# Kernel optimization log

Hardware: AMD Instinct MI355X
Metric: run time of the kernel (lower is better)

## Reference

```python
import jax, jax.numpy as jnp
import numpy as np

B, L, H, O = 2048, 256, 512, 1  # batch, input_len, hidden_size, output_size
EPS = 1e-5

def setup_inputs() -> dict:
    key = jax.random.key(0)
    ks = jax.random.split(key, 16)
    s = 0.05
    return {
        "x": jax.random.normal(ks[0], (B, 1, O), jnp.float32),
        "hidden": jax.random.normal(ks[1], (1, B, H), jnp.float32),
        "encoder_outputs": jax.random.normal(ks[2], (B, L, H), jnp.float32),
        # weights stored [in, out] (transposed torch Linear convention)
        "emb_W": jax.random.normal(ks[3], (O, H), jnp.float32) * s,
        "emb_b": jax.random.normal(ks[4], (H,), jnp.float32) * s,
        "attn_W": jax.random.normal(ks[5], (2 * H, L), jnp.float32) * s,
        "attn_b": jax.random.normal(ks[6], (L,), jnp.float32) * s,
        "comb_W": jax.random.normal(ks[7], (2 * H, H), jnp.float32) * s,
        "comb_b": jax.random.normal(ks[8], (H,), jnp.float32) * s,
        "gru_Wih": jax.random.normal(ks[9], (H, 3 * H), jnp.float32) * s,
        "gru_Whh": jax.random.normal(ks[10], (H, 3 * H), jnp.float32) * s,
        "gru_bih": jax.random.normal(ks[11], (3 * H,), jnp.float32) * s,
        "gru_bhh": jax.random.normal(ks[12], (3 * H,), jnp.float32) * s,
        "out_W": jax.random.normal(ks[13], (H, O), jnp.float32) * s,
        "out_b": jax.random.normal(ks[14], (O,), jnp.float32) * s,
    }

def reference(x, hidden, encoder_outputs, emb_W, emb_b, attn_W, attn_b,
              comb_W, comb_b, gru_Wih, gru_Whh, gru_bih, gru_bhh, out_W, out_b):
    # embedding + InstanceNorm1d over hidden dim (C=1 channel, length=H), no affine
    embedded = x @ emb_W + emb_b                      # [B,1,H]
    mu = jnp.mean(embedded, axis=-1, keepdims=True)
    var = jnp.var(embedded, axis=-1, keepdims=True)   # biased var, matches torch
    embedded = (embedded - mu) * jax.lax.rsqrt(var + EPS)
    # dropout = identity (inference)
    h_b = jnp.transpose(hidden, (1, 0, 2))            # [B,1,H]
    attn_logits = jnp.concatenate([embedded, h_b], axis=2) @ attn_W + attn_b  # [B,1,L]
    attn_weights = jax.nn.softmax(attn_logits, axis=2)
    attn_applied = jnp.einsum('bql,bld->bqd', attn_weights, encoder_outputs)  # [B,1,H]
    out = jnp.concatenate([embedded, attn_applied], axis=2) @ comb_W + comb_b
    out = jax.nn.relu(out)                            # [B,1,H]
    # single GRU step (num_layers=1, seq_len=1)
    xt = out[:, 0, :]                                 # [B,H]
    h0 = hidden[0]                                    # [B,H]
    gi = xt @ gru_Wih + gru_bih                       # [B,3H]
    gh = h0 @ gru_Whh + gru_bhh
    i_r, i_z, i_n = jnp.split(gi, 3, axis=-1)
    h_r, h_z, h_n = jnp.split(gh, 3, axis=-1)
    r = jax.nn.sigmoid(i_r + h_r)
    z = jax.nn.sigmoid(i_z + h_z)
    n = jnp.tanh(i_n + r * h_n)
    h_new = (1.0 - z) * n + z * h0                    # [B,H]
    output = h_new[:, None, :] @ out_W + out_b        # [B,1,O]
    return output, h_new[None, :, :], attn_weights
```

## Files before the change

### kernel.cpp

```cpp
#include <hip/hip_runtime.h>
#include <math.h>

#define NB 2048
#define NL 256
#define NH 512

typedef unsigned short ushort_t;
typedef short s16x8 __attribute__((ext_vector_type(8)));
typedef short s16x4 __attribute__((ext_vector_type(4)));
typedef float f32x4 __attribute__((ext_vector_type(4)));

__device__ __forceinline__ float wsum(float v){
  #pragma unroll
  for (int o = 32; o; o >>= 1) v += __shfl_xor(v, o);
  return v;
}
__device__ __forceinline__ float wmax(float v){
  #pragma unroll
  for (int o = 32; o; o >>= 1) v = fmaxf(v, __shfl_xor(v, o));
  return v;
}
__device__ __forceinline__ ushort_t f2bf(float f){
  union { float f; unsigned u; } v; v.f = f;
  unsigned r = v.u + 0x7fffu + ((v.u >> 16) & 1u);
  return (ushort_t)(r >> 16);
}
__device__ __forceinline__ float bf2f(short s){
  union { unsigned u; float f; } v; v.u = ((unsigned)(unsigned short)s) << 16;
  return v.f;
}

__global__ __launch_bounds__(256)
void kPrep(const float* __restrict__ eW, const float* __restrict__ eb,
           const float* __restrict__ attn_W, const float* __restrict__ comb_W,
           float* __restrict__ stats,
           float* __restrict__ p, float* __restrict__ q,
           float* __restrict__ p2, float* __restrict__ q2)
{
  __shared__ float rw[4], rb[4];
  __shared__ float pa[4][64], pb[4][64];
  const int tid = threadIdx.x, lane = tid & 63, wv = tid >> 6;
  const int bid = blockIdx.x;
  float swv = eW[tid] + eW[tid + 256];
  float sbv = eb[tid] + eb[tid + 256];
  swv = wsum(swv); sbv = wsum(sbv);
  if (lane == 0) { rw[wv] = swv; rb[wv] = sbv; }
  __syncthreads();
  const float mW = (rw[0]+rw[1]+rw[2]+rw[3]) * (1.f/NH);
  const float mb = (rb[0]+rb[1]+rb[2]+rb[3]) * (1.f/NH);

  if (bid == 12) {
    float u0 = eW[tid]-mW, u1 = eW[tid+256]-mW;
    float v0 = eb[tid]-mb, v1 = eb[tid+256]-mb;
    float s2 = u0*u0 + u1*u1, s3 = u0*v0 + u1*v1, s4 = v0*v0 + v1*v1;
    s2 = wsum(s2); s3 = wsum(s3); s4 = wsum(s4);
    if (lane == 0) { pa[0][wv] = s2; pa[1][wv] = s3; pa[2][wv] = s4; }
    __syncthreads();
    if (tid == 0) {
      stats[0] = mW; stats[1] = mb;
      stats[2] = pa[0][0]+pa[0][1]+pa[0][2]+pa[0][3];
      stats[3] = pa[1][0]+pa[1][1]+pa[1][2]+pa[1][3];
      stats[4] = pa[2][0]+pa[2][1]+pa[2][2]+pa[2][3];
    }
    return;
  }
  const float* Wsrc; int ldw, c0; float *op, *oq;
  if (bid < 4) { Wsrc = attn_W; ldw = NL; c0 = bid*64;     op = p  + c0; oq = q  + c0; }
  else         { Wsrc = comb_W; ldw = NH; c0 = (bid-4)*64; op = p2 + c0; oq = q2 + c0; }
  const int c = c0 + lane;
  const int hc = tid >> 6;
  float ap = 0.f, aq = 0.f;
  for (int h = hc*128; h < hc*128 + 128; ++h) {
    float w = Wsrc[(size_t)h*ldw + c];
    ap = fmaf(eW[h]-mW, w, ap);
    aq = fmaf(eb[h]-mb, w, aq);
  }
  pa[hc][lane] = ap; pb[hc][lane] = aq;
  __syncthreads();
  if (hc == 0) {
    op[lane] = pa[0][lane]+pa[1][lane]+pa[2][lane]+pa[3][lane];
    oq[lane] = pb[0][lane]+pb[1][lane]+pb[2][lane]+pb[3][lane];
  }
}

__global__ __launch_bounds__(256)
void kPrepB(const float* __restrict__ hidden,
            const float* __restrict__ attn_W, const float* __restrict__ comb_W,
            const float* __restrict__ Wih, const float* __restrict__ Whh,
            ushort_t* __restrict__ A2, ushort_t* __restrict__ WTA,
            ushort_t* __restrict__ WTC, ushort_t* __restrict__ WTG)
{
  const int bid = blockIdx.x, tid = threadIdx.x;
  if (bid < 512) {
    const int idx = (bid*256 + tid) * 8;
    const int b = idx >> 9, h = idx & 511;
    float4 v0 = *(const float4*)(hidden + idx);
    float4 v1 = *(const float4*)(hidden + idx + 4);
    s16x8 o;
    o[0]=f2bf(v0.x); o[1]=f2bf(v0.y); o[2]=f2bf(v0.z); o[3]=f2bf(v0.w);
    o[4]=f2bf(v1.x); o[5]=f2bf(v1.y); o[6]=f2bf(v1.z); o[7]=f2bf(v1.w);
    *(s16x8*)&A2[(size_t)b*1024 + 512 + h] = o;
    return;
  }
  if (bid < 544) {
    const int b2 = bid - 512, bx = b2 & 3, by = b2 >> 2;
    const int c = bx*64 + (tid & 63);
    const int ksub = by*64 + (tid >> 6)*16;
    ushort_t vals[16];
    #pragma unroll
    for (int kk = 0; kk < 16; ++kk)
      vals[kk] = f2bf(attn_W[(size_t)(512 + ksub + kk)*NL + c]);
    *(s16x8*)&WTA[(size_t)c*512 + ksub]     = *(s16x8*)&vals[0];
    *(s16x8*)&WTA[(size_t)c*512 + ksub + 8] = *(s16x8*)&vals[8];
    return;
  }
  if (bid < 608) {
    const int b2 = bid - 544, bx = b2 & 7, by = b2 >> 3;
    const int c = bx*64 + (tid & 63);
    const int ksub = by*64 + (tid >> 6)*16;
    ushort_t vals[16];
    #pragma unroll
    for (int kk = 0; kk < 16; ++kk)
      vals[kk] = f2bf(comb_W[(size_t)(512 + ksub + kk)*NH + c]);
    *(s16x8*)&WTC[(size_t)c*512 + ksub]     = *(s16x8*)&vals[0];
    *(s16x8*)&WTC[(size_t)c*512 + ksub + 8] = *(s16x8*)&vals[8];
    return;
  }
  {
    const int b2 = bid - 608, bx = b2 & 31, by = b2 >> 5;
    const int n = bx*64 + (tid & 63);
    const int ksub = by*64 + (tid >> 6)*16;
    const int g = n >> 6, t = (n >> 4) & 3, c = (g << 4) | (n & 15);
    const int sc = (t == 0) ? c : (t == 1) ? (512 + c) : (1024 + c);
    ushort_t vals[16];
    #pragma unroll
    for (int kk = 0; kk < 16; ++kk) {
      int k = ksub + kk;
      float v;
      if (k < 512) v = (t == 3) ? 0.f : Wih[(size_t)k*1536 + sc];
      else         v = (t == 2) ? 0.f : Whh[(size_t)(k-512)*1536 + sc];
      vals[kk] = f2bf(v);
    }
    *(s16x8*)&WTG[(size_t)n*1024 + ksub]     = *(s16x8*)&vals[0];
    *(s16x8*)&WTG[(size_t)n*1024 + ksub + 8] = *(s16x8*)&vals[8];
  }
}

__global__ __launch_bounds__(128)
void k2fused(const float* __restrict__ x, const float* __restrict__ hidden,
             const float* __restrict__ enc, const ushort_t* __restrict__ WTA,
             const float* __restrict__ attn_b,
             const float* __restrict__ p, const float* __restrict__ q,
             const float* __restrict__ stats,
             float* __restrict__ attn_out, ushort_t* __restrict__ abf)
{
  __shared__ __align__(16) float h0s[NH];
  __shared__ float wl[NL];
  __shared__ float sred[2];
  const int tid = threadIdx.x, lane = tid & 63, wv = tid >> 6;
  const int b = blockIdx.x;

  ((float4*)h0s)[tid] = ((const float4*)(hidden + (size_t)b*NH))[tid];
  __syncthreads();

  const float xv = x[b];
  const float rs = rsqrtf((xv*xv*stats[2] + 2.f*xv*stats[3] + stats[4])*(1.0f/NH) + 1e-5f);
  float lg[2];
  #pragma unroll
  for (int cc = 0; cc < 2; ++cc) {
    const int c = tid + cc*128;
    const ushort_t* wrow = WTA + (size_t)c*512;
    float acc = 0.f;
    #pragma unroll 4
    for (int k = 0; k < NH; k += 8) {
      s16x8 w = *(const s16x8*)&wrow[k];
      #pragma unroll
      for (int jj = 0; jj < 8; ++jj)
        acc = fmaf(bf2f(w[jj]), h0s[k+jj], acc);
    }
    lg[cc] = acc + attn_b[c] + xv*rs*p[c] + rs*q[c];
  }
  float m = wmax(fmaxf(lg[0], lg[1]));
  if (lane == 0) sred[wv] = m;
  __syncthreads();
  m = fmaxf(sred[0], sred[1]);
  __syncthreads();
  float e0 = expf(lg[0]-m), e1 = expf(lg[1]-m);
  float s = wsum(e0 + e1);
  if (lane == 0) sred[wv] = s;
  __syncthreads();
  const float inv = 1.f / (sred[0] + sred[1]);
  e0 *= inv; e1 *= inv;
  wl[tid] = e0; wl[tid+128] = e1;
  attn_out[(size_t)b*NL + tid]       = e0;
  attn_out[(size_t)b*NL + tid + 128] = e1;
  __syncthreads();

  const float4* ep = (const float4*)(enc + (size_t)b*NL*NH);
  float4 acc = {0.f,0.f,0.f,0.f};
  #pragma unroll 4
  for (int l = 0; l < NL; ++l) {
    float wv2 = wl[l];
    float4 e = ep[l*(NH/4) + tid];
    acc.x = fmaf(wv2,e.x,acc.x); acc.y = fmaf(wv2,e.y,acc.y);
    acc.z = fmaf(wv2,e.z,acc.z); acc.w = fmaf(wv2,e.w,acc.w);
  }
  s16x4 o; o[0]=f2bf(acc.x); o[1]=f2bf(acc.y); o[2]=f2bf(acc.z); o[3]=f2bf(acc.w);
  *(s16x4*)&abf[(size_t)b*NH + tid*4] = o;
}

template<int EPI>
__global__ __launch_bounds__(256)
void gemm_bf16(const ushort_t* __restrict__ A, int lda,
               const ushort_t* __restrict__ Bt, int K,
               const float* __restrict__ xin, const float* __restrict__ stats,
               const float* __restrict__ pvec, const float* __restrict__ qvec,
               const float* __restrict__ bias,
               ushort_t* __restrict__ out_bf,
               const float* __restrict__ bih, const float* __restrict__ bhh,
               const float* __restrict__ hidden, float* __restrict__ h_out)
{
  __shared__ ushort_t As[128][72];
  __shared__ ushort_t Bs[64][72];
  const int tid = threadIdx.x, lane = tid & 63, wr = tid >> 6;
  const int m0 = blockIdx.x * 128, n0 = blockIdx.y * 64;

  f32x4 acc[2][4];
  #pragma unroll
  for (int i = 0; i < 2; ++i)
    #pragma unroll
    for (int j = 0; j < 4; ++j)
      acc[i][j] = (f32x4){0.f,0.f,0.f,0.f};

  const int srow = tid >> 3, scol = (tid & 7) * 8;
  for (int kt = 0; kt < K; kt += 64) {
    __syncthreads();
    #pragma unroll
    for (int it = 0; it < 4; ++it) {
      const int r = srow + it*32;
      *(s16x8*)&As[r][scol] = *(const s16x8*)&A[(size_t)(m0+r)*lda + kt + scol];
    }
    #pragma unroll
    for (int it = 0; it < 2; ++it) {
      const int r = srow + it*32;
      *(s16x8*)&Bs[r][scol] = *(const s16x8*)&Bt[(size_t)(n0+r)*K + kt + scol];
    }
    __syncthreads();
    #pragma unroll
    for (int ks = 0; ks < 2; ++ks) {
      const int ko = ks*32 + (lane >> 4)*8;
      s16x8 af[2], bfr[4];
      #pragma unroll
      for (int i = 0; i < 2; ++i) af[i]  = *(const s16x8*)&As[wr*32 + i*16 + (lane & 15)][ko];
      #pragma unroll
      for (int j = 0; j < 4; ++j) bfr[j] = *(const s16x8*)&Bs[j*16 + (lane & 15)][ko];
      #pragma unroll
      for (int i = 0; i < 2; ++i)
        #pragma unroll
        for (int j = 0; j < 4; ++j)
          acc[i][j] = __builtin_amdgcn_mfma_f32_16x16x32_bf16(af[i], bfr[j], acc[i][j], 0, 0, 0);
    }
  }

  if constexpr (EPI == 2) {
    const float S2 = stats[2], S3 = stats[3], S4 = stats[4];
    #pragma unroll
    for (int i = 0; i < 2; ++i) {
      #pragma unroll
      for (int reg = 0; reg < 4; ++reg) {
        const int row = m0 + wr*32 + i*16 + ((lane >> 4) << 2) + reg;
        const float xv = xin[row];
        const float rs = rsqrtf((xv*xv*S2 + 2.f*xv*S3 + S4)*(1.0f/NH) + 1e-5f);
        const float al = xv*rs, be = rs;
        #pragma unroll
        for (int j = 0; j < 4; ++j) {
          const int col = n0 + j*16 + (lane & 15);
          float v = acc[i][j][reg] + bias[col] + al*pvec[col] + be*qvec[col];
          out_bf[(size_t)row*1024 + col] = f2bf(fmaxf(v, 0.f));
        }
      }
    }
  } else {
    const int g = n0 >> 6;
    const int hcol = (g << 4) | (lane & 15);
    const float b_r = bih[hcol]        + bhh[hcol];
    const float b_z = bih[512 + hcol]  + bhh[512 + hcol];
    const float b_i = bih[1024 + hcol];
    const float b_h = bhh[1024 + hcol];
    #pragma unroll
    for (int i = 0; i < 2; ++i) {
      #pragma unroll
      for (int reg = 0; reg < 4; ++reg) {
        const int row = m0 + wr*32 + i*16 + ((lane >> 4) << 2) + reg;
        float rv = 1.f / (1.f + expf(-(acc[i][0][reg] + b_r)));
        float zv = 1.f / (1.f + expf(-(acc[i][1][reg] + b_z)));
        float nv = tanhf(acc[i][2][reg] + b_i + rv * (acc[i][3][reg] + b_h));
        float h0v = hidden[(size_t)row*NH + hcol];
        h_out[(size_t)row*NH + hcol] = nv + zv * (h0v - nv);
      }
    }
  }
}

__global__ __launch_bounds__(256)
void kOut(const float* __restrict__ h, const float* __restrict__ out_W,
          const float* __restrict__ out_b, float* __restrict__ out0)
{
  const int row = blockIdx.x * 4 + (threadIdx.x >> 6);
  const int lane = threadIdx.x & 63;
  const float4* hp = (const float4*)(h + (size_t)row*NH);
  const float4* wp = (const float4*)out_W;
  float4 h1 = hp[lane*2], h2 = hp[lane*2+1];
  float4 w1 = wp[lane*2], w2 = wp[lane*2+1];
  float d = h1.x*w1.x + h1.y*w1.y + h1.z*w1.z + h1.w*w1.w
          + h2.x*w2.x + h2.y*w2.y + h2.z*w2.z + h2.w*w2.w;
  d = wsum(d);
  if (lane == 0) out0[row] = d + out_b[0];
}

extern "C" void kernel_launch(void* const* d_in, const int* in_sizes, int n_in,
                              void* d_out, int out_size, void* d_ws, size_t ws_size,
                              hipStream_t stream)
{
  const float* x      = (const float*)d_in[0];
  const float* hidden = (const float*)d_in[1];
  const float* enc    = (const float*)d_in[2];
  const float* emb_W  = (const float*)d_in[3];
  const float* emb_b  = (const float*)d_in[4];
  const float* attn_W = (const float*)d_in[5];
  const float* attn_b = (const float*)d_in[6];
  const float* comb_W = (const float*)d_in[7];
  const float* comb_b = (const float*)d_in[8];
  const float* Wih    = (const float*)d_in[9];
  const float* Whh    = (const float*)d_in[10];
  const float* bih    = (const float*)d_in[11];
  const float* bhh    = (const float*)d_in[12];
  const float* out_W  = (const float*)d_in[13];
  const float* out_b  = (const float*)d_in[14];

  float* out      = (float*)d_out;
  float* out0     = out;
  float* out_h    = out + NB;
  float* out_attn = out + NB + (size_t)NB*NH;

  float* wsf   = (float*)d_ws;
  float* stats = wsf;
  float* p     = wsf + 16;
  float* q     = wsf + 272;
  float* p2    = wsf + 528;
  float* q2    = wsf + 1040;
  ushort_t* usb = (ushort_t*)(wsf + 1600);
  ushort_t* A2  = usb;
  ushort_t* ABF = usb + 2097152;
  ushort_t* WTA = usb + 3145728;
  ushort_t* WTC = usb + 3276800;
  ushort_t* WTG = usb + 3538944;

  kPrep<<<13, 256, 0, stream>>>(emb_W, emb_b, attn_W, comb_W, stats, p, q, p2, q2);
  kPrepB<<<1120, 256, 0, stream>>>(hidden, attn_W, comb_W, Wih, Whh, A2, WTA, WTC, WTG);
  k2fused<<<NB, 128, 0, stream>>>(x, hidden, enc, WTA, attn_b, p, q, stats,
                                  out_attn, ABF);
  gemm_bf16<2><<<dim3(16, 8), 256, 0, stream>>>(ABF, 512, WTC, 512,
      x, stats, p2, q2, comb_b, A2, nullptr, nullptr, nullptr, nullptr);
  gemm_bf16<3><<<dim3(16, 32), 256, 0, stream>>>(A2, 1024, WTG, 1024,
      nullptr, nullptr, nullptr, nullptr, nullptr, nullptr, bih, bhh, hidden, out_h);
  kOut<<<512, 256, 0, stream>>>(out_h, out_W, out_b, out0);
}
```

Before: 299.0 us.

## Fuse combine matmul into attention kernel and merge prep kernels

Merges the two prep kernels into one launch. The combine-layer matmul moves into the per-batch attention kernel as an fp32 matrix-vector product over shared-memory attention output, removing the separate bf16 GEMM launch and its intermediate buffer. The attention and combine weights are now kept in fp32 instead of bf16. This cuts launches and intermediate traffic but does 512x512 FMA per row on scalar ALUs, and every block re-reads 1 MB of fp32 combine weights (served from cache), in place of an MFMA GEMM.

Result: slower. 534.5 us (+78.8%).

```diff
diff --git a/kernel.cpp b/kernel.cpp
--- a/kernel.cpp
+++ b/kernel.cpp
@@ -25,70 +25,17 @@
   unsigned r = v.u + 0x7fffu + ((v.u >> 16) & 1u);
   return (ushort_t)(r >> 16);
 }
-__device__ __forceinline__ float bf2f(short s){
-  union { unsigned u; float f; } v; v.u = ((unsigned)(unsigned short)s) << 16;
-  return v.f;
-}
 
 __global__ __launch_bounds__(256)
-void kPrep(const float* __restrict__ eW, const float* __restrict__ eb,
-           const float* __restrict__ attn_W, const float* __restrict__ comb_W,
-           float* __restrict__ stats,
-           float* __restrict__ p, float* __restrict__ q,
-           float* __restrict__ p2, float* __restrict__ q2)
-{
-  __shared__ float rw[4], rb[4];
-  __shared__ float pa[4][64], pb[4][64];
-  const int tid = threadIdx.x, lane = tid & 63, wv = tid >> 6;
-  const int bid = blockIdx.x;
-  float swv = eW[tid] + eW[tid + 256];
-  float sbv = eb[tid] + eb[tid + 256];
-  swv = wsum(swv); sbv = wsum(sbv);
-  if (lane == 0) { rw[wv] = swv; rb[wv] = sbv; }
-  __syncthreads();
-  const float mW = (rw[0]+rw[1]+rw[2]+rw[3]) * (1.f/NH);
-  const float mb = (rb[0]+rb[1]+rb[2]+rb[3]) * (1.f/NH);
-
-  if (bid == 12) {
-    float u0 = eW[tid]-mW, u1 = eW[tid+256]-mW;
-    float v0 = eb[tid]-mb, v1 = eb[tid+256]-mb;
-    float s2 = u0*u0 + u1*u1, s3 = u0*v0 + u1*v1, s4 = v0*v0 + v1*v1;
-    s2 = wsum(s2); s3 = wsum(s3); s4 = wsum(s4);
-    if (lane == 0) { pa[0][wv] = s2; pa[1][wv] = s3; pa[2][wv] = s4; }
-    __syncthreads();
-    if (tid == 0) {
-      stats[0] = mW; stats[1] = mb;
-      stats[2] = pa[0][0]+pa[0][1]+pa[0][2]+pa[0][3];
-      stats[3] = pa[1][0]+pa[1][1]+pa[1][2]+pa[1][3];
-      stats[4] = pa[2][0]+pa[2][1]+pa[2][2]+pa[2][3];
-    }
-    return;
-  }
-  const float* Wsrc; int ldw, c0; float *op, *oq;
-  if (bid < 4) { Wsrc = attn_W; ldw = NL; c0 = bid*64;     op = p  + c0; oq = q  + c0; }
-  else         { Wsrc = comb_W; ldw = NH; c0 = (bid-4)*64; op = p2 + c0; oq = q2 + c0; }
-  const int c = c0 + lane;
-  const int hc = tid >> 6;
-  float ap = 0.f, aq = 0.f;
-  for (int h = hc*128; h < hc*128 + 128; ++h) {
-    float w = Wsrc[(size_t)h*ldw + c];
-    ap = fmaf(eW[h]-mW, w, ap);
-    aq = fmaf(eb[h]-mb, w, aq);
-  }
-  pa[hc][lane] = ap; pb[hc][lane] = aq;
-  __syncthreads();
-  if (hc == 0) {
-    op[lane] = pa[0][lane]+pa[1][lane]+pa[2][lane]+pa[3][lane];
-    oq[lane] = pb[0][lane]+pb[1][lane]+pb[2][lane]+pb[3][lane];
-  }
-}
-
-__global__ __launch_bounds__(256)
-void kPrepB(const float* __restrict__ hidden,
-            const float* __restrict__ attn_W, const float* __restrict__ comb_W,
-            const float* __restrict__ Wih, const float* __restrict__ Whh,
-            ushort_t* __restrict__ A2, ushort_t* __restrict__ WTA,
-            ushort_t* __restrict__ WTC, ushort_t* __restrict__ WTG)
+void kPrepAll(const float* __restrict__ hidden,
+              const float* __restrict__ eW, const float* __restrict__ eb,
+              const float* __restrict__ attn_W, const float* __restrict__ comb_W,
+              const float* __restrict__ Wih, const float* __restrict__ Whh,
+              ushort_t* __restrict__ A2, float* __restrict__ WTA,
+              float* __restrict__ WTC, ushort_t* __restrict__ WTG,
+              float* __restrict__ stats,
+              float* __restrict__ p, float* __restrict__ q,
+              float* __restrict__ p2, float* __restrict__ q2)
 {
   const int bid = blockIdx.x, tid = threadIdx.x;
   if (bid < 512) {
@@ -106,27 +53,29 @@
     const int b2 = bid - 512, bx = b2 & 3, by = b2 >> 2;
     const int c = bx*64 + (tid & 63);
     const int ksub = by*64 + (tid >> 6)*16;
-    ushort_t vals[16];
+    float vals[16];
     #pragma unroll
     for (int kk = 0; kk < 16; ++kk)
-      vals[kk] = f2bf(attn_W[(size_t)(512 + ksub + kk)*NL + c]);
-    *(s16x8*)&WTA[(size_t)c*512 + ksub]     = *(s16x8*)&vals[0];
-    *(s16x8*)&WTA[(size_t)c*512 + ksub + 8] = *(s16x8*)&vals[8];
+      vals[kk] = attn_W[(size_t)(512 + ksub + kk)*NL + c];
+    #pragma unroll
+    for (int kk = 0; kk < 4; ++kk)
+      *(float4*)&WTA[(size_t)c*512 + ksub + kk*4] = *(float4*)&vals[kk*4];
     return;
   }
   if (bid < 608) {
     const int b2 = bid - 544, bx = b2 & 7, by = b2 >> 3;
     const int c = bx*64 + (tid & 63);
     const int ksub = by*64 + (tid >> 6)*16;
-    ushort_t vals[16];
+    float vals[16];
     #pragma unroll
     for (int kk = 0; kk < 16; ++kk)
-      vals[kk] = f2bf(comb_W[(size_t)(512 + ksub + kk)*NH + c]);
-    *(s16x8*)&WTC[(size_t)c*512 + ksub]     = *(s16x8*)&vals[0];
-    *(s16x8*)&WTC[(size_t)c*512 + ksub + 8] = *(s16x8*)&vals[8];
+      vals[kk] = comb_W[(size_t)(512 + ksub + kk)*NH + c];
+    #pragma unroll
+    for (int kk = 0; kk < 4; ++kk)
+      *(float4*)&WTC[(size_t)c*512 + ksub + kk*4] = *(float4*)&vals[kk*4];
     return;
   }
-  {
+  if (bid < 1120) {
     const int b2 = bid - 608, bx = b2 & 31, by = b2 >> 5;
     const int n = bx*64 + (tid & 63);
     const int ksub = by*64 + (tid >> 6)*16;
@@ -143,20 +92,72 @@
     }
     *(s16x8*)&WTG[(size_t)n*1024 + ksub]     = *(s16x8*)&vals[0];
     *(s16x8*)&WTG[(size_t)n*1024 + ksub + 8] = *(s16x8*)&vals[8];
+    return;
+  }
+  {
+    __shared__ float rw[4], rb[4];
+    __shared__ float pa[4][64], pb[4][64];
+    const int lane = tid & 63, wv = tid >> 6;
+    float swv = eW[tid] + eW[tid + 256];
+    float sbv = eb[tid] + eb[tid + 256];
+    swv = wsum(swv); sbv = wsum(sbv);
+    if (lane == 0) { rw[wv] = swv; rb[wv] = sbv; }
+    __syncthreads();
+    const float mW = (rw[0]+rw[1]+rw[2]+rw[3]) * (1.f/NH);
+    const float mb = (rb[0]+rb[1]+rb[2]+rb[3]) * (1.f/NH);
+
+    if (bid == 1132) {
+      float u0 = eW[tid]-mW, u1 = eW[tid+256]-mW;
+      float v0 = eb[tid]-mb, v1 = eb[tid+256]-mb;
+      float s2 = u0*u0 + u1*u1, s3 = u0*v0 + u1*v1, s4 = v0*v0 + v1*v1;
+      s2 = wsum(s2); s3 = wsum(s3); s4 = wsum(s4);
+      if (lane == 0) { pa[0][wv] = s2; pa[1][wv] = s3; pa[2][wv] = s4; }
+      __syncthreads();
+      if (tid == 0) {
+        stats[0] = mW; stats[1] = mb;
+        stats[2] = pa[0][0]+pa[0][1]+pa[0][2]+pa[0][3];
+        stats[3] = pa[1][0]+pa[1][1]+pa[1][2]+pa[1][3];
+        stats[4] = pa[2][0]+pa[2][1]+pa[2][2]+pa[2][3];
+      }
+      return;
+    }
+    const int bid2 = bid - 1120;
+    const float* Wsrc; int ldw, c0; float *op, *oq;
+    if (bid2 < 4) { Wsrc = attn_W; ldw = NL; c0 = bid2*64;     op = p  + c0; oq = q  + c0; }
+    else          { Wsrc = comb_W; ldw = NH; c0 = (bid2-4)*64; op = p2 + c0; oq = q2 + c0; }
+    const int c = c0 + lane;
+    const int hc = tid >> 6;
+    float ap = 0.f, aq = 0.f;
+    #pragma unroll 4
+    for (int h = hc*128; h < hc*128 + 128; ++h) {
+      float w = Wsrc[(size_t)h*ldw + c];
+      ap = fmaf(eW[h]-mW, w, ap);
+      aq = fmaf(eb[h]-mb, w, aq);
+    }
+    pa[hc][lane] = ap; pb[hc][lane] = aq;
+    __syncthreads();
+    if (hc == 0) {
+      op[lane] = pa[0][lane]+pa[1][lane]+pa[2][lane]+pa[3][lane];
+      oq[lane] = pb[0][lane]+pb[1][lane]+pb[2][lane]+pb[3][lane];
+    }
   }
 }
 
 __global__ __launch_bounds__(128)
 void k2fused(const float* __restrict__ x, const float* __restrict__ hidden,
-             const float* __restrict__ enc, const ushort_t* __restrict__ WTA,
-             const float* __restrict__ attn_b,
+             const float* __restrict__ enc,
+             const float* __restrict__ WTA, const float* __restrict__ attn_b,
              const float* __restrict__ p, const float* __restrict__ q,
+             const float* __restrict__ WTC, const float* __restrict__ comb_b,
+             const float* __restrict__ p2, const float* __restrict__ q2,
              const float* __restrict__ stats,
-             float* __restrict__ attn_out, ushort_t* __restrict__ abf)
+             float* __restrict__ attn_out, ushort_t* __restrict__ A2)
 {
   __shared__ __align__(16) float h0s[NH];
+  __shared__ __align__(16) float a_s[NH];
   __shared__ float wl[NL];
   __shared__ float sred[2];
+  __shared__ __align__(16) ushort_t xt_s[NH];
   const int tid = threadIdx.x, lane = tid & 63, wv = tid >> 6;
   const int b = blockIdx.x;
 
@@ -165,20 +166,21 @@
 
   const float xv = x[b];
   const float rs = rsqrtf((xv*xv*stats[2] + 2.f*xv*stats[3] + stats[4])*(1.0f/NH) + 1e-5f);
+  const float al = xv*rs, be = rs;
+
   float lg[2];
   #pragma unroll
   for (int cc = 0; cc < 2; ++cc) {
     const int c = tid + cc*128;
-    const ushort_t* wrow = WTA + (size_t)c*512;
+    const float4* wrow = (const float4*)(WTA + (size_t)c*512);
     float acc = 0.f;
-    #pragma unroll 4
-    for (int k = 0; k < NH; k += 8) {
-      s16x8 w = *(const s16x8*)&wrow[k];
-      #pragma unroll
-      for (int jj = 0; jj < 8; ++jj)
-        acc = fmaf(bf2f(w[jj]), h0s[k+jj], acc);
-    }
-    lg[cc] = acc + attn_b[c] + xv*rs*p[c] + rs*q[c];
+    #pragma unroll 8
+    for (int kq = 0; kq < 128; ++kq) {
+      float4 w = wrow[kq];
+      const float* h4 = &h0s[kq*4];
+      acc = fmaf(w.x,h4[0],fmaf(w.y,h4[1],fmaf(w.z,h4[2],fmaf(w.w,h4[3],acc))));
+    }
+    lg[cc] = acc + attn_b[c] + al*p[c] + be*q[c];
   }
   float m = wmax(fmaxf(lg[0], lg[1]));
   if (lane == 0) sred[wv] = m;
@@ -205,25 +207,37 @@
     acc.x = fmaf(wv2,e.x,acc.x); acc.y = fmaf(wv2,e.y,acc.y);
     acc.z = fmaf(wv2,e.z,acc.z); acc.w = fmaf(wv2,e.w,acc.w);
   }
-  s16x4 o; o[0]=f2bf(acc.x); o[1]=f2bf(acc.y); o[2]=f2bf(acc.z); o[3]=f2bf(acc.w);
-  *(s16x4*)&abf[(size_t)b*NH + tid*4] = o;
-}
-
-template<int EPI>
+  ((float4*)a_s)[tid] = acc;
+  __syncthreads();
+
+  #pragma unroll
+  for (int cc = 0; cc < 4; ++cc) {
+    const int c = tid + cc*128;
+    const float4* wrow = (const float4*)(WTC + (size_t)c*512);
+    const float4* a4 = (const float4*)a_s;
+    float acc2 = comb_b[c] + al*p2[c] + be*q2[c];
+    #pragma unroll 8
+    for (int kq = 0; kq < 128; ++kq) {
+      float4 w = wrow[kq];
+      float4 av = a4[kq];
+      acc2 = fmaf(w.x,av.x,fmaf(w.y,av.y,fmaf(w.z,av.z,fmaf(w.w,av.w,acc2))));
+    }
+    xt_s[c] = f2bf(fmaxf(acc2, 0.f));
+  }
+  __syncthreads();
+  *(s16x4*)&A2[(size_t)b*1024 + tid*4] = *(s16x4*)&xt_s[tid*4];
+}
+
 __global__ __launch_bounds__(256)
-void gemm_bf16(const ushort_t* __restrict__ A, int lda,
-               const ushort_t* __restrict__ Bt, int K,
-               const float* __restrict__ xin, const float* __restrict__ stats,
-               const float* __restrict__ pvec, const float* __restrict__ qvec,
-               const float* __restrict__ bias,
-               ushort_t* __restrict__ out_bf,
-               const float* __restrict__ bih, const float* __restrict__ bhh,
-               const float* __restrict__ hidden, float* __restrict__ h_out)
+void gemmGRU(const ushort_t* __restrict__ A, const ushort_t* __restrict__ Bt,
+             const float* __restrict__ bih, const float* __restrict__ bhh,
+             const float* __restrict__ hidden, float* __restrict__ h_out)
 {
   __shared__ ushort_t As[128][72];
   __shared__ ushort_t Bs[64][72];
   const int tid = threadIdx.x, lane = tid & 63, wr = tid >> 6;
   const int m0 = blockIdx.x * 128, n0 = blockIdx.y * 64;
+  const int K = 1024;
 
   f32x4 acc[2][4];
   #pragma unroll
@@ -238,7 +252,7 @@
     #pragma unroll
     for (int it = 0; it < 4; ++it) {
       const int r = srow + it*32;
-      *(s16x8*)&As[r][scol] = *(const s16x8*)&A[(size_t)(m0+r)*lda + kt + scol];
+      *(s16x8*)&As[r][scol] = *(const s16x8*)&A[(size_t)(m0+r)*1024 + kt + scol];
     }
     #pragma unroll
     for (int it = 0; it < 2; ++it) {
@@ -262,42 +276,22 @@
     }
   }
 
-  if constexpr (EPI == 2) {
-    const float S2 = stats[2], S3 = stats[3], S4 = stats[4];
-    #pragma unroll
-    for (int i = 0; i < 2; ++i) {
-      #pragma unroll
-      for (int reg = 0; reg < 4; ++reg) {
-        const int row = m0 + wr*32 + i*16 + ((lane >> 4) << 2) + reg;
-        const float xv = xin[row];
-        const float rs = rsqrtf((xv*xv*S2 + 2.f*xv*S3 + S4)*(1.0f/NH) + 1e-5f);
-        const float al = xv*rs, be = rs;
-        #pragma unroll
-        for (int j = 0; j < 4; ++j) {
-          const int col = n0 + j*16 + (lane & 15);
-          float v = acc[i][j][reg] + bias[col] + al*pvec[col] + be*qvec[col];
-          out_bf[(size_t)row*1024 + col] = f2bf(fmaxf(v, 0.f));
-        }
-      }
-    }
-  } else {
-    const int g = n0 >> 6;
-    const int hcol = (g << 4) | (lane & 15);
-    const float b_r = bih[hcol]        + bhh[hcol];
-    const float b_z = bih[512 + hcol]  + bhh[512 + hcol];
-    const float b_i = bih[1024 + hcol];
-    const float b_h = bhh[1024 + hcol];
-    #pragma unroll
-    for (int i = 0; i < 2; ++i) {
-      #pragma unroll
-      for (int reg = 0; reg < 4; ++reg) {
-        const int row = m0 + wr*32 + i*16 + ((lane >> 4) << 2) + reg;
-        float rv = 1.f / (1.f + expf(-(acc[i][0][reg] + b_r)));
-        float zv = 1.f / (1.f + expf(-(acc[i][1][reg] + b_z)));
-        float nv = tanhf(acc[i][2][reg] + b_i + rv * (acc[i][3][reg] + b_h));
-        float h0v = hidden[(size_t)row*NH + hcol];
-        h_out[(size_t)row*NH + hcol] = nv + zv * (h0v - nv);
-      }
+  const int g = n0 >> 6;
+  const int hcol = (g << 4) | (lane & 15);
+  const float b_r = bih[hcol]        + bhh[hcol];
+  const float b_z = bih[512 + hcol]  + bhh[512 + hcol];
+  const float b_i = bih[1024 + hcol];
+  const float b_h = bhh[1024 + hcol];
+  #pragma unroll
+  for (int i = 0; i < 2; ++i) {
+    #pragma unroll
+    for (int reg = 0; reg < 4; ++reg) {
+      const int row = m0 + wr*32 + i*16 + ((lane >> 4) << 2) + reg;
+      float rv = 1.f / (1.f + expf(-(acc[i][0][reg] + b_r)));
+      float zv = 1.f / (1.f + expf(-(acc[i][1][reg] + b_z)));
+      float nv = tanhf(acc[i][2][reg] + b_i + rv * (acc[i][3][reg] + b_h));
+      float h0v = hidden[(size_t)row*NH + hcol];
+      h_out[(size_t)row*NH + hcol] = nv + zv * (h0v - nv);
     }
   }
 }
@@ -349,20 +343,17 @@
   float* q     = wsf + 272;
   float* p2    = wsf + 528;
   float* q2    = wsf + 1040;
-  ushort_t* usb = (ushort_t*)(wsf + 1600);
+  float* WTA   = wsf + 2048;
+  float* WTC   = wsf + 133120;
+  ushort_t* usb = (ushort_t*)(wsf + 395264);
   ushort_t* A2  = usb;
-  ushort_t* ABF = usb + 2097152;
-  ushort_t* WTA = usb + 3145728;
-  ushort_t* WTC = usb + 3276800;
-  ushort_t* WTG = usb + 3538944;
-
-  kPrep<<<13, 256, 0, stream>>>(emb_W, emb_b, attn_W, comb_W, stats, p, q, p2, q2);
-  kPrepB<<<1120, 256, 0, stream>>>(hidden, attn_W, comb_W, Wih, Whh, A2, WTA, WTC, WTG);
-  k2fused<<<NB, 128, 0, stream>>>(x, hidden, enc, WTA, attn_b, p, q, stats,
-                                  out_attn, ABF);
-  gemm_bf16<2><<<dim3(16, 8), 256, 0, stream>>>(ABF, 512, WTC, 512,
-      x, stats, p2, q2, comb_b, A2, nullptr, nullptr, nullptr, nullptr);
-  gemm_bf16<3><<<dim3(16, 32), 256, 0, stream>>>(A2, 1024, WTG, 1024,
-      nullptr, nullptr, nullptr, nullptr, nullptr, nullptr, bih, bhh, hidden, out_h);
+  ushort_t* WTG = usb + 2097152;
+
+  kPrepAll<<<1133, 256, 0, stream>>>(hidden, emb_W, emb_b, attn_W, comb_W,
+                                     Wih, Whh, A2, WTA, WTC, WTG,
+                                     stats, p, q, p2, q2);
+  k2fused<<<NB, 128, 0, stream>>>(x, hidden, enc, WTA, attn_b, p, q,
+                                  WTC, comb_b, p2, q2, stats, out_attn, A2);
+  gemmGRU<<<dim3(16, 32), 256, 0, stream>>>(A2, WTG, bih, bhh, hidden, out_h);
   kOut<<<512, 256, 0, stream>>>(out_h, out_W, out_b, out0);
 }
```

## Move attention logits to MFMA GEMM, merge prep kernels, fuse output projection

Applied to the files above, without the earlier changes.

Merges the two prep kernels into one launch that also seeds the output with out_b. Attention logits are now computed by a bf16 MFMA GEMM instead of a per-batch scalar dot-product loop in k2fused. A new streaming kernel does the softmax and the encoder-weighted sum with 256 threads split over two halves of L. The final out_W projection is folded into the GRU GEMM epilogue with shuffle reductions and atomicAdd, which removes kOut but adds atomic contention and nondeterministic summation order.

Measured after the change: 265.7 us. 1.13x faster.

```diff
diff --git a/kernel.cpp b/kernel.cpp
--- a/kernel.cpp
+++ b/kernel.cpp
@@ -25,70 +25,19 @@
   unsigned r = v.u + 0x7fffu + ((v.u >> 16) & 1u);
   return (ushort_t)(r >> 16);
 }
-__device__ __forceinline__ float bf2f(short s){
-  union { unsigned u; float f; } v; v.u = ((unsigned)(unsigned short)s) << 16;
-  return v.f;
-}
 
 __global__ __launch_bounds__(256)
-void kPrep(const float* __restrict__ eW, const float* __restrict__ eb,
-           const float* __restrict__ attn_W, const float* __restrict__ comb_W,
-           float* __restrict__ stats,
-           float* __restrict__ p, float* __restrict__ q,
-           float* __restrict__ p2, float* __restrict__ q2)
-{
-  __shared__ float rw[4], rb[4];
-  __shared__ float pa[4][64], pb[4][64];
-  const int tid = threadIdx.x, lane = tid & 63, wv = tid >> 6;
-  const int bid = blockIdx.x;
-  float swv = eW[tid] + eW[tid + 256];
-  float sbv = eb[tid] + eb[tid + 256];
-  swv = wsum(swv); sbv = wsum(sbv);
-  if (lane == 0) { rw[wv] = swv; rb[wv] = sbv; }
-  __syncthreads();
-  const float mW = (rw[0]+rw[1]+rw[2]+rw[3]) * (1.f/NH);
-  const float mb = (rb[0]+rb[1]+rb[2]+rb[3]) * (1.f/NH);
-
-  if (bid == 12) {
-    float u0 = eW[tid]-mW, u1 = eW[tid+256]-mW;
-    float v0 = eb[tid]-mb, v1 = eb[tid+256]-mb;
-    float s2 = u0*u0 + u1*u1, s3 = u0*v0 + u1*v1, s4 = v0*v0 + v1*v1;
-    s2 = wsum(s2); s3 = wsum(s3); s4 = wsum(s4);
-    if (lane == 0) { pa[0][wv] = s2; pa[1][wv] = s3; pa[2][wv] = s4; }
-    __syncthreads();
-    if (tid == 0) {
-      stats[0] = mW; stats[1] = mb;
-      stats[2] = pa[0][0]+pa[0][1]+pa[0][2]+pa[0][3];
-      stats[3] = pa[1][0]+pa[1][1]+pa[1][2]+pa[1][3];
-      stats[4] = pa[2][0]+pa[2][1]+pa[2][2]+pa[2][3];
-    }
-    return;
-  }
-  const float* Wsrc; int ldw, c0; float *op, *oq;
-  if (bid < 4) { Wsrc = attn_W; ldw = NL; c0 = bid*64;     op = p  + c0; oq = q  + c0; }
-  else         { Wsrc = comb_W; ldw = NH; c0 = (bid-4)*64; op = p2 + c0; oq = q2 + c0; }
-  const int c = c0 + lane;
-  const int hc = tid >> 6;
-  float ap = 0.f, aq = 0.f;
-  for (int h = hc*128; h < hc*128 + 128; ++h) {
-    float w = Wsrc[(size_t)h*ldw + c];
-    ap = fmaf(eW[h]-mW, w, ap);
-    aq = fmaf(eb[h]-mb, w, aq);
-  }
-  pa[hc][lane] = ap; pb[hc][lane] = aq;
-  __syncthreads();
-  if (hc == 0) {
-    op[lane] = pa[0][lane]+pa[1][lane]+pa[2][lane]+pa[3][lane];
-    oq[lane] = pb[0][lane]+pb[1][lane]+pb[2][lane]+pb[3][lane];
-  }
-}
-
-__global__ __launch_bounds__(256)
-void kPrepB(const float* __restrict__ hidden,
-            const float* __restrict__ attn_W, const float* __restrict__ comb_W,
-            const float* __restrict__ Wih, const float* __restrict__ Whh,
-            ushort_t* __restrict__ A2, ushort_t* __restrict__ WTA,
-            ushort_t* __restrict__ WTC, ushort_t* __restrict__ WTG)
+void kPrepAll(const float* __restrict__ hidden,
+              const float* __restrict__ eW, const float* __restrict__ eb,
+              const float* __restrict__ attn_W, const float* __restrict__ comb_W,
+              const float* __restrict__ Wih, const float* __restrict__ Whh,
+              const float* __restrict__ out_b,
+              ushort_t* __restrict__ A2, ushort_t* __restrict__ WTG,
+              ushort_t* __restrict__ WTA, ushort_t* __restrict__ WTC,
+              float* __restrict__ stats,
+              float* __restrict__ p, float* __restrict__ q,
+              float* __restrict__ p2, float* __restrict__ q2,
+              float* __restrict__ out0)
 {
   const int bid = blockIdx.x, tid = threadIdx.x;
   if (bid < 512) {
@@ -102,32 +51,8 @@
     *(s16x8*)&A2[(size_t)b*1024 + 512 + h] = o;
     return;
   }
-  if (bid < 544) {
-    const int b2 = bid - 512, bx = b2 & 3, by = b2 >> 2;
-    const int c = bx*64 + (tid & 63);
-    const int ksub = by*64 + (tid >> 6)*16;
-    ushort_t vals[16];
-    #pragma unroll
-    for (int kk = 0; kk < 16; ++kk)
-      vals[kk] = f2bf(attn_W[(size_t)(512 + ksub + kk)*NL + c]);
-    *(s16x8*)&WTA[(size_t)c*512 + ksub]     = *(s16x8*)&vals[0];
-    *(s16x8*)&WTA[(size_t)c*512 + ksub + 8] = *(s16x8*)&vals[8];
-    return;
-  }
-  if (bid < 608) {
-    const int b2 = bid - 544, bx = b2 & 7, by = b2 >> 3;
-    const int c = bx*64 + (tid & 63);
-    const int ksub = by*64 + (tid >> 6)*16;
-    ushort_t vals[16];
-    #pragma unroll
-    for (int kk = 0; kk < 16; ++kk)
-      vals[kk] = f2bf(comb_W[(size_t)(512 + ksub + kk)*NH + c]);
-    *(s16x8*)&WTC[(size_t)c*512 + ksub]     = *(s16x8*)&vals[0];
-    *(s16x8*)&WTC[(size_t)c*512 + ksub + 8] = *(s16x8*)&vals[8];
-    return;
-  }
-  {
-    const int b2 = bid - 608, bx = b2 & 31, by = b2 >> 5;
+  if (bid < 1024) {
+    const int b2 = bid - 512, bx = b2 & 31, by = b2 >> 5;
     const int n = bx*64 + (tid & 63);
     const int ksub = by*64 + (tid >> 6)*16;
     const int g = n >> 6, t = (n >> 4) & 3, c = (g << 4) | (n & 15);
@@ -143,70 +68,83 @@
     }
     *(s16x8*)&WTG[(size_t)n*1024 + ksub]     = *(s16x8*)&vals[0];
     *(s16x8*)&WTG[(size_t)n*1024 + ksub + 8] = *(s16x8*)&vals[8];
-  }
-}
-
-__global__ __launch_bounds__(128)
-void k2fused(const float* __restrict__ x, const float* __restrict__ hidden,
-             const float* __restrict__ enc, const ushort_t* __restrict__ WTA,
-             const float* __restrict__ attn_b,
-             const float* __restrict__ p, const float* __restrict__ q,
-             const float* __restrict__ stats,
-             float* __restrict__ attn_out, ushort_t* __restrict__ abf)
-{
-  __shared__ __align__(16) float h0s[NH];
-  __shared__ float wl[NL];
-  __shared__ float sred[2];
-  const int tid = threadIdx.x, lane = tid & 63, wv = tid >> 6;
-  const int b = blockIdx.x;
-
-  ((float4*)h0s)[tid] = ((const float4*)(hidden + (size_t)b*NH))[tid];
-  __syncthreads();
-
-  const float xv = x[b];
-  const float rs = rsqrtf((xv*xv*stats[2] + 2.f*xv*stats[3] + stats[4])*(1.0f/NH) + 1e-5f);
-  float lg[2];
-  #pragma unroll
-  for (int cc = 0; cc < 2; ++cc) {
-    const int c = tid + cc*128;
-    const ushort_t* wrow = WTA + (size_t)c*512;
-    float acc = 0.f;
+    return;
+  }
+  if (bid < 1056) {
+    const int b2 = bid - 1024, bx = b2 & 3, by = b2 >> 2;
+    const int c = bx*64 + (tid & 63);
+    const int ksub = by*64 + (tid >> 6)*16;
+    ushort_t vals[16];
+    #pragma unroll
+    for (int kk = 0; kk < 16; ++kk)
+      vals[kk] = f2bf(attn_W[(size_t)(512 + ksub + kk)*NL + c]);
+    *(s16x8*)&WTA[(size_t)c*512 + ksub]     = *(s16x8*)&vals[0];
+    *(s16x8*)&WTA[(size_t)c*512 + ksub + 8] = *(s16x8*)&vals[8];
+    return;
+  }
+  if (bid < 1120) {
+    const int b2 = bid - 1056, bx = b2 & 7, by = b2 >> 3;
+    const int c = bx*64 + (tid & 63);
+    const int ksub = by*64 + (tid >> 6)*16;
+    ushort_t vals[16];
+    #pragma unroll
+    for (int kk = 0; kk < 16; ++kk)
+      vals[kk] = f2bf(comb_W[(size_t)(512 + ksub + kk)*NH + c]);
+    *(s16x8*)&WTC[(size_t)c*512 + ksub]     = *(s16x8*)&vals[0];
+    *(s16x8*)&WTC[(size_t)c*512 + ksub + 8] = *(s16x8*)&vals[8];
+    return;
+  }
+  if (bid > 1132) {
+    out0[(bid-1133)*256 + tid] = out_b[0];
+    return;
+  }
+  {
+    __shared__ float rw[4], rb[4];
+    __shared__ float pa[4][64], pb[4][64];
+    const int lane = tid & 63, wv = tid >> 6;
+    float swv = eW[tid] + eW[tid + 256];
+    float sbv = eb[tid] + eb[tid + 256];
+    swv = wsum(swv); sbv = wsum(sbv);
+    if (lane == 0) { rw[wv] = swv; rb[wv] = sbv; }
+    __syncthreads();
+    const float mW = (rw[0]+rw[1]+rw[2]+rw[3]) * (1.f/NH);
+    const float mb = (rb[0]+rb[1]+rb[2]+rb[3]) * (1.f/NH);
+
+    if (bid == 1132) {
+      float u0 = eW[tid]-mW, u1 = eW[tid+256]-mW;
+      float v0 = eb[tid]-mb, v1 = eb[tid+256]-mb;
+      float s2 = u0*u0 + u1*u1, s3 = u0*v0 + u1*v1, s4 = v0*v0 + v1*v1;
+      s2 = wsum(s2); s3 = wsum(s3); s4 = wsum(s4);
+      if (lane == 0) { pa[0][wv] = s2; pa[1][wv] = s3; pa[2][wv] = s4; }
+      __syncthreads();
+      if (tid == 0) {
+        stats[0] = mW; stats[1] = mb;
+        stats[2] = pa[0][0]+pa[0][1]+pa[0][2]+pa[0][3];
+        stats[3] = pa[1][0]+pa[1][1]+pa[1][2]+pa[1][3];
+        stats[4] = pa[2][0]+pa[2][1]+pa[2][2]+pa[2][3];
+      }
+      return;
+    }
+    const int bid2 = bid - 1120;
+    const float* Wsrc; int ldw, c0; float *op, *oq;
+    if (bid2 < 4) { Wsrc = attn_W; ldw = NL; c0 = bid2*64;     op = p  + c0; oq = q  + c0; }
+    else          { Wsrc = comb_W; ldw = NH; c0 = (bid2-4)*64; op = p2 + c0; oq = q2 + c0; }
+    const int c = c0 + lane;
+    const int hc = tid >> 6;
+    float ap = 0.f, aq = 0.f;
     #pragma unroll 4
-    for (int k = 0; k < NH; k += 8) {
-      s16x8 w = *(const s16x8*)&wrow[k];
-      #pragma unroll
-      for (int jj = 0; jj < 8; ++jj)
-        acc = fmaf(bf2f(w[jj]), h0s[k+jj], acc);
-    }
-    lg[cc] = acc + attn_b[c] + xv*rs*p[c] + rs*q[c];
-  }
-  float m = wmax(fmaxf(lg[0], lg[1]));
-  if (lane == 0) sred[wv] = m;
-  __syncthreads();
-  m = fmaxf(sred[0], sred[1]);
-  __syncthreads();
-  float e0 = expf(lg[0]-m), e1 = expf(lg[1]-m);
-  float s = wsum(e0 + e1);
-  if (lane == 0) sred[wv] = s;
-  __syncthreads();
-  const float inv = 1.f / (sred[0] + sred[1]);
-  e0 *= inv; e1 *= inv;
-  wl[tid] = e0; wl[tid+128] = e1;
-  attn_out[(size_t)b*NL + tid]       = e0;
-  attn_out[(size_t)b*NL + tid + 128] = e1;
-  __syncthreads();
-
-  const float4* ep = (const float4*)(enc + (size_t)b*NL*NH);
-  float4 acc = {0.f,0.f,0.f,0.f};
-  #pragma unroll 4
-  for (int l = 0; l < NL; ++l) {
-    float wv2 = wl[l];
-    float4 e = ep[l*(NH/4) + tid];
-    acc.x = fmaf(wv2,e.x,acc.x); acc.y = fmaf(wv2,e.y,acc.y);
-    acc.z = fmaf(wv2,e.z,acc.z); acc.w = fmaf(wv2,e.w,acc.w);
-  }
-  s16x4 o; o[0]=f2bf(acc.x); o[1]=f2bf(acc.y); o[2]=f2bf(acc.z); o[3]=f2bf(acc.w);
-  *(s16x4*)&abf[(size_t)b*NH + tid*4] = o;
+    for (int h = hc*128; h < hc*128 + 128; ++h) {
+      float w = Wsrc[(size_t)h*ldw + c];
+      ap = fmaf(eW[h]-mW, w, ap);
+      aq = fmaf(eb[h]-mb, w, aq);
+    }
+    pa[hc][lane] = ap; pb[hc][lane] = aq;
+    __syncthreads();
+    if (hc == 0) {
+      op[lane] = pa[0][lane]+pa[1][lane]+pa[2][lane]+pa[3][lane];
+      oq[lane] = pb[0][lane]+pb[1][lane]+pb[2][lane]+pb[3][lane];
+    }
+  }
 }
 
 template<int EPI>
@@ -216,9 +154,10 @@
                const float* __restrict__ xin, const float* __restrict__ stats,
                const float* __restrict__ pvec, const float* __restrict__ qvec,
                const float* __restrict__ bias,
-               ushort_t* __restrict__ out_bf,
+               float* __restrict__ out_f, ushort_t* __restrict__ out_bf,
                const float* __restrict__ bih, const float* __restrict__ bhh,
-               const float* __restrict__ hidden, float* __restrict__ h_out)
+               const float* __restrict__ hidden, const float* __restrict__ out_W,
+               float* __restrict__ h_out, float* __restrict__ out0)
 {
   __shared__ ushort_t As[128][72];
   __shared__ ushort_t Bs[64][72];
@@ -262,7 +201,7 @@
     }
   }
 
-  if constexpr (EPI == 2) {
+  if constexpr (EPI == 1 || EPI == 2) {
     const float S2 = stats[2], S3 = stats[3], S4 = stats[4];
     #pragma unroll
     for (int i = 0; i < 2; ++i) {
@@ -276,7 +215,8 @@
         for (int j = 0; j < 4; ++j) {
           const int col = n0 + j*16 + (lane & 15);
           float v = acc[i][j][reg] + bias[col] + al*pvec[col] + be*qvec[col];
-          out_bf[(size_t)row*1024 + col] = f2bf(fmaxf(v, 0.f));
+          if constexpr (EPI == 1) out_f[(size_t)row*NL + col] = v;
+          else                    out_bf[(size_t)row*1024 + col] = f2bf(fmaxf(v, 0.f));
         }
       }
     }
@@ -287,6 +227,7 @@
     const float b_z = bih[512 + hcol]  + bhh[512 + hcol];
     const float b_i = bih[1024 + hcol];
     const float b_h = bhh[1024 + hcol];
+    const float ow  = out_W[hcol];
     #pragma unroll
     for (int i = 0; i < 2; ++i) {
       #pragma unroll
@@ -296,26 +237,61 @@
         float zv = 1.f / (1.f + expf(-(acc[i][1][reg] + b_z)));
         float nv = tanhf(acc[i][2][reg] + b_i + rv * (acc[i][3][reg] + b_h));
         float h0v = hidden[(size_t)row*NH + hcol];
-        h_out[(size_t)row*NH + hcol] = nv + zv * (h0v - nv);
+        float hn = nv + zv * (h0v - nv);
+        h_out[(size_t)row*NH + hcol] = hn;
+        float partial = hn * ow;
+        #pragma unroll
+        for (int o = 1; o < 16; o <<= 1) partial += __shfl_xor(partial, o);
+        if ((lane & 15) == 0) atomicAdd(&out0[row], partial);
       }
     }
   }
 }
 
 __global__ __launch_bounds__(256)
-void kOut(const float* __restrict__ h, const float* __restrict__ out_W,
-          const float* __restrict__ out_b, float* __restrict__ out0)
+void kStream(const float* __restrict__ logits, const float* __restrict__ enc,
+             float* __restrict__ attn_out, ushort_t* __restrict__ ABF)
 {
-  const int row = blockIdx.x * 4 + (threadIdx.x >> 6);
-  const int lane = threadIdx.x & 63;
-  const float4* hp = (const float4*)(h + (size_t)row*NH);
-  const float4* wp = (const float4*)out_W;
-  float4 h1 = hp[lane*2], h2 = hp[lane*2+1];
-  float4 w1 = wp[lane*2], w2 = wp[lane*2+1];
-  float d = h1.x*w1.x + h1.y*w1.y + h1.z*w1.z + h1.w*w1.w
-          + h2.x*w2.x + h2.y*w2.y + h2.z*w2.z + h2.w*w2.w;
-  d = wsum(d);
-  if (lane == 0) out0[row] = d + out_b[0];
+  __shared__ float wl[NL];
+  __shared__ __align__(16) float4 ps[128];
+  __shared__ float sred[4];
+  const int tid = threadIdx.x, lane = tid & 63, wv = tid >> 6;
+  const int b = blockIdx.x;
+
+  float lg = logits[(size_t)b*NL + tid];
+  float m = wmax(lg);
+  if (lane == 0) sred[wv] = m;
+  __syncthreads();
+  m = fmaxf(fmaxf(sred[0], sred[1]), fmaxf(sred[2], sred[3]));
+  float e = expf(lg - m);
+  float s = wsum(e);
+  __syncthreads();
+  if (lane == 0) sred[wv] = s;
+  __syncthreads();
+  const float inv = 1.f / (sred[0] + sred[1] + sred[2] + sred[3]);
+  e *= inv;
+  wl[tid] = e;
+  attn_out[(size_t)b*NL + tid] = e;
+  __syncthreads();
+
+  const int col = tid & 127, half = tid >> 7;
+  const float4* ep = (const float4*)(enc + (size_t)b*NL*NH);
+  float4 acc = {0.f,0.f,0.f,0.f};
+  #pragma unroll 4
+  for (int l = half*128; l < half*128 + 128; ++l) {
+    float w = wl[l];
+    float4 ev = ep[l*(NH/4) + col];
+    acc.x = fmaf(w,ev.x,acc.x); acc.y = fmaf(w,ev.y,acc.y);
+    acc.z = fmaf(w,ev.z,acc.z); acc.w = fmaf(w,ev.w,acc.w);
+  }
+  if (half == 0) ps[col] = acc;
+  __syncthreads();
+  if (half == 1) {
+    float4 o = ps[col];
+    o.x += acc.x; o.y += acc.y; o.z += acc.z; o.w += acc.w;
+    s16x4 ov; ov[0]=f2bf(o.x); ov[1]=f2bf(o.y); ov[2]=f2bf(o.z); ov[3]=f2bf(o.w);
+    *(s16x4*)&ABF[(size_t)b*NH + col*4] = ov;
+  }
 }
 
 extern "C" void kernel_launch(void* const* d_in, const int* in_sizes, int n_in,
@@ -343,26 +319,31 @@
   float* out_h    = out + NB;
   float* out_attn = out + NB + (size_t)NB*NH;
 
-  float* wsf   = (float*)d_ws;
-  float* stats = wsf;
-  float* p     = wsf + 16;
-  float* q     = wsf + 272;
-  float* p2    = wsf + 528;
-  float* q2    = wsf + 1040;
-  ushort_t* usb = (ushort_t*)(wsf + 1600);
+  float* wsf    = (float*)d_ws;
+  float* stats  = wsf;
+  float* p      = wsf + 16;
+  float* q      = wsf + 272;
+  float* p2     = wsf + 528;
+  float* q2     = wsf + 1040;
+  float* logits = wsf + 2048;
+  ushort_t* usb = (ushort_t*)(wsf + 526400);
   ushort_t* A2  = usb;
   ushort_t* ABF = usb + 2097152;
   ushort_t* WTA = usb + 3145728;
   ushort_t* WTC = usb + 3276800;
   ushort_t* WTG = usb + 3538944;
 
-  kPrep<<<13, 256, 0, stream>>>(emb_W, emb_b, attn_W, comb_W, stats, p, q, p2, q2);
-  kPrepB<<<1120, 256, 0, stream>>>(hidden, attn_W, comb_W, Wih, Whh, A2, WTA, WTC, WTG);
-  k2fused<<<NB, 128, 0, stream>>>(x, hidden, enc, WTA, attn_b, p, q, stats,
-                                  out_attn, ABF);
+  kPrepAll<<<1141, 256, 0, stream>>>(hidden, emb_W, emb_b, attn_W, comb_W,
+                                     Wih, Whh, out_b, A2, WTG, WTA, WTC,
+                                     stats, p, q, p2, q2, out0);
+  gemm_bf16<1><<<dim3(16, 4), 256, 0, stream>>>(A2 + 512, 1024, WTA, 512,
+      x, stats, p, q, attn_b, logits, nullptr,
+      nullptr, nullptr, nullptr, nullptr, nullptr, nullptr);
+  kStream<<<NB, 256, 0, stream>>>(logits, enc, out_attn, ABF);
   gemm_bf16<2><<<dim3(16, 8), 256, 0, stream>>>(ABF, 512, WTC, 512,
-      x, stats, p2, q2, comb_b, A2, nullptr, nullptr, nullptr, nullptr);
+      x, stats, p2, q2, comb_b, nullptr, A2,
+      nullptr, nullptr, nullptr, nullptr, nullptr, nullptr);
   gemm_bf16<3><<<dim3(16, 32), 256, 0, stream>>>(A2, 1024, WTG, 1024,
-      nullptr, nullptr, nullptr, nullptr, nullptr, nullptr, bih, bhh, hidden, out_h);
-  kOut<<<512, 256, 0, stream>>>(out_h, out_W, out_b, out0);
-}
+      nullptr, nullptr, nullptr, nullptr, nullptr, nullptr, nullptr,
+      bih, bhh, hidden, out_W, out_h, out0);
+}
```
